# Performance work log

Measured on AMD Instinct MI355X. Metric: run time of the kernel, lower is better.

Reference implementation:

```python
import jax, jax.numpy as jnp
import numpy as np

N_COG = 72  # 360 / delta_cog
N_RB = 72   # 360 / delta_rb
B, N, H = 64, 512, 128


def setup_inputs() -> dict:
    key = jax.random.key(0)
    k1, k2, k3, k4, k5, k6 = jax.random.split(key, 6)
    h_t = jax.random.normal(k1, (N, B, H), dtype=jnp.float32)
    r_mat = jax.random.randint(k2, (B, N, N), 0, N_RB, dtype=jnp.int32)
    d_mat = jax.random.uniform(k3, (B, N, N), dtype=jnp.float32)
    mask = jax.random.randint(k4, (B, N), 0, 2).astype(jnp.float32)
    cog_mat = jax.random.randint(k5, (B, N, N), 0, N_COG, dtype=jnp.int32)
    domain = jax.random.normal(k6, (N_COG, N_RB), dtype=jnp.float32)
    return {"h_t": h_t, "r_mat": r_mat, "d_mat": d_mat, "mask": mask,
            "cog_mat": cog_mat, "domain": domain}


def reference(h_t, r_mat, d_mat, mask, cog_mat, domain):
    # gather from learnable domain table, subtract distance, relu
    w = jax.nn.relu(domain[cog_mat, r_mat] - d_mat)          # [B, N, N]
    # pairwise mask (applied twice in the original, around normalization)
    m = mask[:, :, None] * mask[:, None, :]                   # [B, N, N]
    w = m * w
    # global-max normalize; torch uses .data.max() (no grad through max)
    w = w / jax.lax.stop_gradient(jnp.max(w))
    w = m * w
    # out[b,i,h] = sum_j w[b,i,j] * h_t[j,b,h]
    return jnp.einsum('bij,jbh->bih', w, h_t)                 # [B, N, H]
```

## Files before the change

kernel.cpp:

```cpp
#include <hip/hip_runtime.h>


#define B_   64
#define N_   512
#define H_   128
#define NCOG 72
#define NRB  72

typedef __bf16 bf16x8 __attribute__((ext_vector_type(8)));
typedef float  f32x4  __attribute__((ext_vector_type(4)));

__global__ __launch_bounds__(256) void k_transpose(const float* __restrict__ ht,
                                                   __bf16* __restrict__ T) {
    __shared__ __bf16 tile[32][136];
    const int jt = blockIdx.x * 32;
    const int b  = blockIdx.y;
    const int t  = threadIdx.x;
    {
        const int jj = t >> 3;
        const int h0 = (t & 7) << 4;
        const float* src = ht + ((size_t)(jt + jj) * B_ + b) * H_ + h0;
        float4 v0 = *(const float4*)(src + 0);
        float4 v1 = *(const float4*)(src + 4);
        float4 v2 = *(const float4*)(src + 8);
        float4 v3 = *(const float4*)(src + 12);
        __bf16* dst = &tile[jj][h0];
        dst[0]=(__bf16)v0.x; dst[1]=(__bf16)v0.y; dst[2]=(__bf16)v0.z; dst[3]=(__bf16)v0.w;
        dst[4]=(__bf16)v1.x; dst[5]=(__bf16)v1.y; dst[6]=(__bf16)v1.z; dst[7]=(__bf16)v1.w;
        dst[8]=(__bf16)v2.x; dst[9]=(__bf16)v2.y; dst[10]=(__bf16)v2.z; dst[11]=(__bf16)v2.w;
        dst[12]=(__bf16)v3.x; dst[13]=(__bf16)v3.y; dst[14]=(__bf16)v3.z; dst[15]=(__bf16)v3.w;
    }
    __syncthreads();
    {
        const int h  = t >> 1;
        const int j0 = (t & 1) << 4;
        union { bf16x8 v[2]; __bf16 e[16]; } ob;
        #pragma unroll
        for (int q = 0; q < 16; ++q) ob.e[q] = tile[j0 + q][h];
        __bf16* dst = T + ((size_t)b * H_ + h) * N_ + jt + j0;
        *(bf16x8*)(dst + 0) = ob.v[0];
        *(bf16x8*)(dst + 8) = ob.v[1];
    }
}

struct Batch { int4 c0, c1, r0, r1; float4 d0, d1; };

__global__ __launch_bounds__(512, 4) void k_main(const int* __restrict__ cog,
                                                 const int* __restrict__ rmat,
                                                 const float* __restrict__ dmat,
                                                 const float* __restrict__ mask,
                                                 const float* __restrict__ domain,
                                                 const __bf16* __restrict__ T,
                                                 float* __restrict__ out,
                                                 unsigned int* __restrict__ gmax) {
    __shared__ float sdom[NCOG * NRB];
    __shared__ float smask[N_];
    __shared__ float sred[4][16][132];
    __shared__ float swmax[8];
    const int b  = blockIdx.y;
    const int i0 = blockIdx.x * 64;
    const int t  = threadIdx.x;
    for (int k = t; k < NCOG * NRB; k += 512) sdom[k] = domain[k];
    for (int k = t; k < N_; k += 512) smask[k] = mask[b * N_ + k];
    __syncthreads();

    const int wave = t >> 6;
    const int lane = t & 63;
    const int quad = lane >> 4;
    const int lrow = lane & 15;
    const int wi   = wave & 3;
    const int kh   = wave >> 2;
    const int irow = i0 + wi * 16 + lrow;
    const size_t rowbase = ((size_t)b * N_ + irow) * N_;
    const int kbeg = kh * 256;

    const int*   cp = cog  + rowbase + kbeg + quad * 8;
    const int*   rp = rmat + rowbase + kbeg + quad * 8;
    const float* dp = dmat + rowbase + kbeg + quad * 8;
    const __bf16* Tb = T + (size_t)b * H_ * N_ + (size_t)lrow * N_ + kbeg + quad * 8;

    f32x4 acc[8];
    #pragma unroll
    for (int i = 0; i < 8; ++i) acc[i] = (f32x4)0.0f;
    float wmax = 0.0f;

    Batch cur, nxt;
    cur.c0 = *(const int4*)(cp);     cur.c1 = *(const int4*)(cp + 4);
    cur.r0 = *(const int4*)(rp);     cur.r1 = *(const int4*)(rp + 4);
    cur.d0 = *(const float4*)(dp);   cur.d1 = *(const float4*)(dp + 4);

    #pragma unroll
    for (int s = 0; s < 8; ++s) {
        const int kk = s * 32;
        bf16x8 bf[8];
        #pragma unroll
        for (int nt = 0; nt < 8; ++nt)
            bf[nt] = *(const bf16x8*)(Tb + kk + (size_t)nt * 16 * N_);
        if (s < 7) {
            nxt.c0 = *(const int4*)(cp + kk + 32);  nxt.c1 = *(const int4*)(cp + kk + 36);
            nxt.r0 = *(const int4*)(rp + kk + 32);  nxt.r1 = *(const int4*)(rp + kk + 36);
            nxt.d0 = *(const float4*)(dp + kk + 32); nxt.d1 = *(const float4*)(dp + kk + 36);
        }
        union { int4 v[2]; int e[8]; } ci, ri;
        union { float4 v[2]; float e[8]; } di;
        ci.v[0] = cur.c0; ci.v[1] = cur.c1;
        ri.v[0] = cur.r0; ri.v[1] = cur.r1;
        di.v[0] = cur.d0; di.v[1] = cur.d1;
        const int jb = kbeg + kk + quad * 8;
        union { bf16x8 v8; __bf16 e[8]; } af;
        #pragma unroll
        for (int q = 0; q < 8; ++q) {
            float val = sdom[ci.e[q] * NRB + ri.e[q]] - di.e[q];
            val = fmaxf(val, 0.0f) * smask[jb + q];
            wmax = fmaxf(wmax, val);
            af.e[q] = (__bf16)val;
        }
        #pragma unroll
        for (int nt = 0; nt < 8; ++nt)
            acc[nt] = __builtin_amdgcn_mfma_f32_16x16x32_bf16(af.v8, bf[nt], acc[nt], 0, 0, 0);
        cur = nxt;
    }
    wmax *= smask[irow];

    #pragma unroll
    for (int off = 32; off > 0; off >>= 1)
        wmax = fmaxf(wmax, __shfl_down(wmax, off));
    if (lane == 0) swmax[wave] = wmax;

    if (kh == 1) {
        #pragma unroll
        for (int nt = 0; nt < 8; ++nt)
            #pragma unroll
            for (int r = 0; r < 4; ++r)
                sred[wi][quad * 4 + r][nt * 16 + lrow] = acc[nt][r];
    }
    __syncthreads();

    if (t == 0) {
        float m = swmax[0];
        #pragma unroll
        for (int w = 1; w < 8; ++w) m = fmaxf(m, swmax[w]);
        atomicMax(gmax, __float_as_uint(m));
    }

    if (kh == 0) {
        const int orow0 = i0 + wi * 16 + quad * 4;
        #pragma unroll
        for (int nt = 0; nt < 8; ++nt) {
            #pragma unroll
            for (int r = 0; r < 4; ++r) {
                float v = acc[nt][r] + sred[wi][quad * 4 + r][nt * 16 + lrow];
                out[((size_t)b * N_ + orow0 + r) * H_ + nt * 16 + lrow] = v;
            }
        }
    }
}

__global__ __launch_bounds__(256) void k_scale(float* __restrict__ out,
                                               const float* __restrict__ mask,
                                               const unsigned int* __restrict__ gmax) {
    const float inv = 1.0f / __uint_as_float(*gmax);
    const int idx = blockIdx.x * 256 + threadIdx.x;
    const float m = mask[idx >> 5] * inv;
    float4* p = (float4*)out;
    float4 v = p[idx];
    v.x *= m; v.y *= m; v.z *= m; v.w *= m;
    p[idx] = v;
}

extern "C" void kernel_launch(void* const* d_in, const int* in_sizes, int n_in,
                              void* d_out, int out_size, void* d_ws, size_t ws_size,
                              hipStream_t stream) {
    const float* ht     = (const float*)d_in[0];
    const int*   rmat   = (const int*)  d_in[1];
    const float* dmat   = (const float*)d_in[2];
    const float* mask   = (const float*)d_in[3];
    const int*   cog    = (const int*)  d_in[4];
    const float* domain = (const float*)d_in[5];
    float* out = (float*)d_out;

    unsigned int* gmax = (unsigned int*)d_ws;
    __bf16* T = (__bf16*)((char*)d_ws + 256);

    hipMemsetAsync(d_ws, 0, 256, stream);
    k_transpose<<<dim3(16, 64), 256, 0, stream>>>(ht, T);
    k_main<<<dim3(8, 64), 512, 0, stream>>>(cog, rmat, dmat, mask, domain, T, out, gmax);
    k_scale<<<4096, 256, 0, stream>>>(out, mask, gmax);
}
```

Before: 251.2 us.

## Warp-specialize main kernel with async LDS producer waves and XCD-aware block mapping

```diff
diff --git a/kernel.cpp b/kernel.cpp
--- a/kernel.cpp
+++ b/kernel.cpp
@@ -9,6 +9,12 @@
 
 typedef __bf16 bf16x8 __attribute__((ext_vector_type(8)));
 typedef float  f32x4  __attribute__((ext_vector_type(4)));
+
+__device__ __forceinline__ void async_copy16(const void* g, void* l) {
+    __builtin_amdgcn_global_load_lds(
+        (const __attribute__((address_space(1))) void*)g,
+        (__attribute__((address_space(3))) void*)l, 16, 0, 0);
+}
 
 __global__ __launch_bounds__(256) void k_transpose(const float* __restrict__ ht,
                                                    __bf16* __restrict__ T) {
@@ -43,8 +49,6 @@
     }
 }
 
-struct Batch { int4 c0, c1, r0, r1; float4 d0, d1; };
-
 __global__ __launch_bounds__(512, 4) void k_main(const int* __restrict__ cog,
                                                  const int* __restrict__ rmat,
                                                  const float* __restrict__ dmat,
@@ -53,106 +57,122 @@
                                                  const __bf16* __restrict__ T,
                                                  float* __restrict__ out,
                                                  unsigned int* __restrict__ gmax) {
+    __shared__ int   tiles[2 * 3 * 2048];
     __shared__ float sdom[NCOG * NRB];
     __shared__ float smask[N_];
-    __shared__ float sred[4][16][132];
     __shared__ float swmax[8];
-    const int b  = blockIdx.y;
-    const int i0 = blockIdx.x * 64;
-    const int t  = threadIdx.x;
+
+    const int id    = blockIdx.x;
+    const int xcd   = id & 7;
+    const int i0idx = (id >> 3) & 7;
+    const int bhi   = id >> 6;
+    const int b     = xcd + 8 * bhi;
+    const int i0    = i0idx * 64;
+
+    const int t    = threadIdx.x;
+    const int wave = t >> 6;
+    const int lane = t & 63;
+
     for (int k = t; k < NCOG * NRB; k += 512) sdom[k] = domain[k];
     for (int k = t; k < N_; k += 512) smask[k] = mask[b * N_ + k];
-    __syncthreads();
-
-    const int wave = t >> 6;
-    const int lane = t & 63;
-    const int quad = lane >> 4;
-    const int lrow = lane & 15;
-    const int wi   = wave & 3;
-    const int kh   = wave >> 2;
-    const int irow = i0 + wi * 16 + lrow;
-    const size_t rowbase = ((size_t)b * N_ + irow) * N_;
-    const int kbeg = kh * 256;
-
-    const int*   cp = cog  + rowbase + kbeg + quad * 8;
-    const int*   rp = rmat + rowbase + kbeg + quad * 8;
-    const float* dp = dmat + rowbase + kbeg + quad * 8;
-    const __bf16* Tb = T + (size_t)b * H_ * N_ + (size_t)lrow * N_ + kbeg + quad * 8;
-
-    f32x4 acc[8];
-    #pragma unroll
-    for (int i = 0; i < 8; ++i) acc[i] = (f32x4)0.0f;
+
+    const size_t robase = ((size_t)b * N_ + i0) * N_;
+
     float wmax = 0.0f;
 
-    Batch cur, nxt;
-    cur.c0 = *(const int4*)(cp);     cur.c1 = *(const int4*)(cp + 4);
-    cur.r0 = *(const int4*)(rp);     cur.r1 = *(const int4*)(rp + 4);
-    cur.d0 = *(const float4*)(dp);   cur.d1 = *(const float4*)(dp + 4);
-
-    #pragma unroll
-    for (int s = 0; s < 8; ++s) {
-        const int kk = s * 32;
-        bf16x8 bf[8];
-        #pragma unroll
-        for (int nt = 0; nt < 8; ++nt)
-            bf[nt] = *(const bf16x8*)(Tb + kk + (size_t)nt * 16 * N_);
-        if (s < 7) {
-            nxt.c0 = *(const int4*)(cp + kk + 32);  nxt.c1 = *(const int4*)(cp + kk + 36);
-            nxt.r0 = *(const int4*)(rp + kk + 32);  nxt.r1 = *(const int4*)(rp + kk + 36);
-            nxt.d0 = *(const float4*)(dp + kk + 32); nxt.d1 = *(const float4*)(dp + kk + 36);
-        }
-        union { int4 v[2]; int e[8]; } ci, ri;
-        union { float4 v[2]; float e[8]; } di;
-        ci.v[0] = cur.c0; ci.v[1] = cur.c1;
-        ri.v[0] = cur.r0; ri.v[1] = cur.r1;
-        di.v[0] = cur.d0; di.v[1] = cur.d1;
-        const int jb = kbeg + kk + quad * 8;
-        union { bf16x8 v8; __bf16 e[8]; } af;
-        #pragma unroll
-        for (int q = 0; q < 8; ++q) {
-            float val = sdom[ci.e[q] * NRB + ri.e[q]] - di.e[q];
-            val = fmaxf(val, 0.0f) * smask[jb + q];
-            wmax = fmaxf(wmax, val);
-            af.e[q] = (__bf16)val;
-        }
-        #pragma unroll
-        for (int nt = 0; nt < 8; ++nt)
-            acc[nt] = __builtin_amdgcn_mfma_f32_16x16x32_bf16(af.v8, bf[nt], acc[nt], 0, 0, 0);
-        cur = nxt;
-    }
-    wmax *= smask[irow];
+    if (wave >= 4) {
+        const int pw   = wave - 4;
+        const int csw4 = ((lane & 7) ^ (lane >> 3)) * 4;
+        const size_t poff = (size_t)(lane >> 3) * N_ + csw4;
+
+        #pragma unroll
+        for (int q6 = 0; q6 < 6; ++q6) {
+            const int q = pw * 6 + q6, a = q >> 3, c8 = q & 7;
+            const size_t goff = robase + (size_t)(c8 * 8) * N_ + poff;
+            const void* g = (a == 0) ? (const void*)(cog + goff)
+                          : (a == 1) ? (const void*)(rmat + goff)
+                                     : (const void*)(dmat + goff);
+            async_copy16(g, &tiles[a * 2048 + c8 * 256]);
+        }
+        __syncthreads();
+        for (int s = 0; s < 16; ++s) {
+            if (s + 1 < 16) {
+                const int kk  = (s + 1) * 32;
+                const int buf = (s + 1) & 1;
+                #pragma unroll
+                for (int q6 = 0; q6 < 6; ++q6) {
+                    const int q = pw * 6 + q6, a = q >> 3, c8 = q & 7;
+                    const size_t goff = robase + (size_t)(c8 * 8) * N_ + kk + poff;
+                    const void* g = (a == 0) ? (const void*)(cog + goff)
+                                  : (a == 1) ? (const void*)(rmat + goff)
+                                             : (const void*)(dmat + goff);
+                    async_copy16(g, &tiles[buf * 6144 + a * 2048 + c8 * 256]);
+                }
+            }
+            __syncthreads();
+        }
+    } else {
+        const int quad = lane >> 4;
+        const int lrow = lane & 15;
+        const int row  = wave * 16 + lrow;
+        const int g0   = (row * 8 + ((quad * 2)     ^ (row & 7))) * 4;
+        const int g1   = (row * 8 + ((quad * 2 + 1) ^ (row & 7))) * 4;
+        const __bf16* Tcol = T + (size_t)b * H_ * N_ + (size_t)lrow * N_ + quad * 8;
+
+        f32x4 acc[8];
+        #pragma unroll
+        for (int i = 0; i < 8; ++i) acc[i] = (f32x4)0.0f;
+
+        __syncthreads();
+        for (int s = 0; s < 16; ++s) {
+            const int kk = s * 32;
+            const int jb = kk + quad * 8;
+            bf16x8 bf[8];
+            #pragma unroll
+            for (int nt = 0; nt < 8; ++nt)
+                bf[nt] = *(const bf16x8*)(Tcol + (size_t)nt * 16 * N_ + kk);
+            const int* tb = tiles + (s & 1) * 6144;
+            union { int4 v[2]; int   e[8]; } ci, ri;
+            union { int4 v[2]; float e[8]; } di;
+            ci.v[0] = *(const int4*)(tb + g0);        ci.v[1] = *(const int4*)(tb + g1);
+            ri.v[0] = *(const int4*)(tb + 2048 + g0); ri.v[1] = *(const int4*)(tb + 2048 + g1);
+            di.v[0] = *(const int4*)(tb + 4096 + g0); di.v[1] = *(const int4*)(tb + 4096 + g1);
+
+            union { bf16x8 v8; __bf16 e[8]; } af;
+            #pragma unroll
+            for (int q = 0; q < 8; ++q) {
+                float val = sdom[ci.e[q] * NRB + ri.e[q]] - di.e[q];
+                val = fmaxf(val, 0.0f) * smask[jb + q];
+                wmax = fmaxf(wmax, val);
+                af.e[q] = (__bf16)val;
+            }
+            #pragma unroll
+            for (int nt = 0; nt < 8; ++nt)
+                acc[nt] = __builtin_amdgcn_mfma_f32_16x16x32_bf16(af.v8, bf[nt], acc[nt], 0, 0, 0);
+            __syncthreads();
+        }
+
+        wmax *= smask[i0 + row];
+
+        const int orow0 = i0 + wave * 16 + quad * 4;
+        #pragma unroll
+        for (int nt = 0; nt < 8; ++nt) {
+            #pragma unroll
+            for (int r = 0; r < 4; ++r)
+                out[((size_t)b * N_ + orow0 + r) * H_ + nt * 16 + lrow] = acc[nt][r];
+        }
+    }
 
     #pragma unroll
     for (int off = 32; off > 0; off >>= 1)
         wmax = fmaxf(wmax, __shfl_down(wmax, off));
     if (lane == 0) swmax[wave] = wmax;
-
-    if (kh == 1) {
-        #pragma unroll
-        for (int nt = 0; nt < 8; ++nt)
-            #pragma unroll
-            for (int r = 0; r < 4; ++r)
-                sred[wi][quad * 4 + r][nt * 16 + lrow] = acc[nt][r];
-    }
     __syncthreads();
-
     if (t == 0) {
         float m = swmax[0];
         #pragma unroll
         for (int w = 1; w < 8; ++w) m = fmaxf(m, swmax[w]);
         atomicMax(gmax, __float_as_uint(m));
-    }
-
-    if (kh == 0) {
-        const int orow0 = i0 + wi * 16 + quad * 4;
-        #pragma unroll
-        for (int nt = 0; nt < 8; ++nt) {
-            #pragma unroll
-            for (int r = 0; r < 4; ++r) {
-                float v = acc[nt][r] + sred[wi][quad * 4 + r][nt * 16 + lrow];
-                out[((size_t)b * N_ + orow0 + r) * H_ + nt * 16 + lrow] = v;
-            }
-        }
     }
 }
 
@@ -184,6 +204,6 @@
 
     hipMemsetAsync(d_ws, 0, 256, stream);
     k_transpose<<<dim3(16, 64), 256, 0, stream>>>(ht, T);
-    k_main<<<dim3(8, 64), 512, 0, stream>>>(cog, rmat, dmat, mask, domain, T, out, gmax);
+    k_main<<<dim3(512), 512, 0, stream>>>(cog, rmat, dmat, mask, domain, T, out, gmax);
     k_scale<<<4096, 256, 0, stream>>>(out, mask, gmax);
 }
```

Result: faster. 239.9 us (-4.5%).
